# Kernel optimization log

Hardware: AMD Instinct MI355X
Metric: run time of the kernel (lower is better)

Reference implementation:

```python
import jax, jax.numpy as jnp
import numpy as np

N_MC = 32
DT = 0.1
HIDDEN = 64
PROSPECTIVE_STEPS = 3
# scan_steps=3 -> first 3 of the hard-coded velocities
VELOCITIES = np.array([[0.2, 0.0], [0.0, 0.2], [0.15, 0.15]], dtype=np.float32)


def linear_interp_1d(x, out_size):
    """F.interpolate(mode='linear', align_corners=False) on last axis. x: [..., N]."""
    n = x.shape[-1]
    scale = n / out_size
    pos = (jnp.arange(out_size, dtype=x.dtype) + 0.5) * scale - 0.5
    pos = jnp.clip(pos, 0.0, n - 1)
    lo = jnp.floor(pos).astype(jnp.int32)
    hi = jnp.minimum(lo + 1, n - 1)
    w = pos - lo.astype(x.dtype)
    return x[..., lo] * (1.0 - w) + x[..., hi] * w


def setup_inputs() -> dict:
    key = jax.random.key(0)
    ks = jax.random.split(key, 8)
    B = 16384
    image = jax.random.uniform(ks[0], (B, 28, 28), dtype=jnp.float32)
    s = 1.0 / np.sqrt(N_MC)
    W_ff = jax.random.normal(ks[1], (N_MC, N_MC), dtype=jnp.float32) * s
    W_fb = jax.random.normal(ks[2], (N_MC, N_MC), dtype=jnp.float32) * s
    W_vel = jax.random.normal(ks[3], (N_MC, 2), dtype=jnp.float32) * s
    Wc1 = jax.random.normal(ks[4], (HIDDEN, 4 * N_MC), dtype=jnp.float32) * (1.0 / np.sqrt(4 * N_MC))
    bc1 = jnp.zeros((HIDDEN,), dtype=jnp.float32)
    Wc2 = jax.random.normal(ks[5], (10, HIDDEN), dtype=jnp.float32) * (1.0 / np.sqrt(HIDDEN))
    bc2 = jnp.zeros((10,), dtype=jnp.float32)
    return {"image": image, "W_ff": W_ff, "W_fb": W_fb, "W_vel": W_vel,
            "Wc1": Wc1, "bc1": bc1, "Wc2": Wc2, "bc2": bc2}


def _column_features(image, W_ff, W_fb, W_vel):
    B = image.shape[0]
    flat = image.reshape(B, -1)                       # [B, 784]
    flat_t = jnp.swapaxes(image, 1, 2).reshape(B, -1)  # transpose(0,1) per image
    sensory = linear_interp_1d(flat, N_MC) * 80.0     # [B, n_mc]
    topdown = linear_interp_1d(flat_t, N_MC) * 40.0   # [B, n_mc]

    r6 = jnp.zeros_like(sensory)                      # reset_state per image
    y_fb = jax.nn.relu(topdown @ W_fb.T)              # top-down feedback drive
    for v in VELOCITIES:                              # fixed 3-step scan
        vel_in = W_vel @ jnp.asarray(v)               # [n_mc]
        for _ in range(PROSPECTIVE_STEPS):            # fixed 3 prospective steps
            pred = r6 @ W_fb.T                        # top-down prediction of sensory drive
            eps_pos = jax.nn.relu(sensory - pred)
            eps_neg = jax.nn.relu(pred - sensory)
            y_ff = jax.nn.relu((eps_pos - eps_neg) @ W_ff.T)
            r6 = r6 + DT * (-r6 + y_ff + y_fb + vel_in)  # leaky L6 integrator
    feature = jnp.concatenate([y_ff, y_fb, r6, eps_pos + eps_neg], axis=-1)  # [B, 4*n_mc]
    return feature


def reference(image, W_ff, W_fb, W_vel, Wc1, bc1, Wc2, bc2):
    feature = jax.lax.stop_gradient(_column_features(image, W_ff, W_fb, W_vel))
    h = jax.nn.gelu(feature @ Wc1.T + bc1, approximate=False)
    logits = h @ Wc2.T + bc2                          # [B, 10]
    return logits
```

## Files before the change

### kernel.cpp

```cpp
#include <hip/hip_runtime.h>
#include <math.h>

typedef float f32x4 __attribute__((ext_vector_type(4)));
typedef float f32x2 __attribute__((ext_vector_type(2)));

#define DOT4(A, B) ((A)[0]*(B)[0] + (A)[1]*(B)[1] + (A)[2]*(B)[2] + (A)[3]*(B)[3])

__global__ __launch_bounds__(256, 4) void mnist_dp3(
    const float* __restrict__ img, const float* __restrict__ Wff,
    const float* __restrict__ Wfb, const float* __restrict__ Wvel,
    const float* __restrict__ Wc1, const float* __restrict__ bc1,
    const float* __restrict__ Wc2, const float* __restrict__ bc2,
    float* __restrict__ out) {
  __shared__ float WffL[32 * 36];
  __shared__ float WfbL[32 * 36];
  __shared__ float uSc[2048];
  __shared__ float snL[8 * 36];
  __shared__ float tdL[8 * 36];
  __shared__ float r6L[8 * 36];
  __shared__ float ftL[8 * 132];
  __shared__ float hLd[8 * 68];
  __shared__ float Wc2L[10 * 68];

  const int t = threadIdx.x;
  const int s = t >> 5, p = t & 31;
  const int sg = blockIdx.x * 8 + s;

  const float pos = 24.5f * (float)p + 11.75f;
  const int lo = (int)pos;
  const float w = pos - (float)lo;
  const int ta = (lo % 28) * 28 + lo / 28;
  const int tb = ((lo + 1) % 28) * 28 + (lo + 1) / 28;
  const float* im = img + (size_t)sg * 784;
  const float a0 = im[lo], a1 = im[lo + 1];
  const float c0 = im[ta], c1 = im[tb];
  const float2 wvp = ((const float2*)Wvel)[p];

  {
    const int rj = t >> 3, c4 = (t & 7) * 4;
    *(f32x4*)(WffL + rj * 36 + c4) = *(const f32x4*)(Wff + rj * 32 + c4);
    *(f32x4*)(WfbL + rj * 36 + c4) = *(const f32x4*)(Wfb + rj * 32 + c4);
  }
  if (t < 160) {
    const int r2 = t >> 4, c2 = (t & 15) * 4;
    *(f32x4*)(Wc2L + r2 * 68 + c2) = *(const f32x4*)(Wc2 + r2 * 64 + c2);
  }
  const float sv = (a0 + (a1 - a0) * w) * 80.0f;
  const float tv = (c0 + (c1 - c0) * w) * 40.0f;
  snL[s * 36 + p] = sv;
  tdL[s * 36 + p] = tv;
  __syncthreads();

  {
    const int i = t >> 3, k0 = (t & 7) * 4;
    float m0 = 0.f, m1 = 0.f, m2 = 0.f, m3 = 0.f;
#pragma unroll
    for (int j = 0; j < 32; ++j) {
      const float a = WffL[i * 36 + j];
      const f32x4 w4 = *(const f32x4*)(WfbL + j * 36 + k0);
      m0 += a * w4[0]; m1 += a * w4[1]; m2 += a * w4[2]; m3 += a * w4[3];
    }
    f32x4 m = {m0, m1, m2, m3};
    *(f32x4*)(uSc + i * 36 + k0) = m;
  }
  __syncthreads();

  const float* Mrow = uSc + p * 36;
  const f32x4 M0 = *(const f32x4*)(Mrow +  0);
  const f32x4 M1 = *(const f32x4*)(Mrow +  4);
  const f32x4 M2 = *(const f32x4*)(Mrow +  8);
  const f32x4 M3 = *(const f32x4*)(Mrow + 12);
  const f32x4 M4 = *(const f32x4*)(Mrow + 16);
  const f32x4 M5 = *(const f32x4*)(Mrow + 20);
  const f32x4 M6 = *(const f32x4*)(Mrow + 24);
  const f32x4 M7 = *(const f32x4*)(Mrow + 28);

  float sf = 0.f, yb = 0.f;
#pragma unroll
  for (int jb = 0; jb < 8; ++jb) {
    const f32x4 s4 = *(const f32x4*)(snL + s * 36 + jb * 4);
    const f32x4 t4 = *(const f32x4*)(tdL + s * 36 + jb * 4);
    const f32x4 f4 = *(const f32x4*)(WffL + p * 36 + jb * 4);
    const f32x4 g4 = *(const f32x4*)(WfbL + p * 36 + jb * 4);
    sf += DOT4(f4, s4);
    yb += DOT4(g4, t4);
  }
  yb = fmaxf(yb, 0.f);

  float r = 0.f, y = 0.f, e = 0.f;
  const float VX[3] = {0.2f, 0.0f, 0.15f};
  const float VY[3] = {0.0f, 0.2f, 0.15f};
#pragma unroll
  for (int v = 0; v < 3; ++v) {
    const float vi = wvp.x * VX[v] + wvp.y * VY[v];
#pragma unroll
    for (int st = 0; st < 3; ++st) {
      r6L[s * 36 + p] = r;
      __builtin_amdgcn_wave_barrier();
      const f32x4 r40 = *(const f32x4*)(r6L + s * 36 +  0);
      const f32x4 r41 = *(const f32x4*)(r6L + s * 36 +  4);
      const f32x4 r42 = *(const f32x4*)(r6L + s * 36 +  8);
      const f32x4 r43 = *(const f32x4*)(r6L + s * 36 + 12);
      const f32x4 r44 = *(const f32x4*)(r6L + s * 36 + 16);
      const f32x4 r45 = *(const f32x4*)(r6L + s * 36 + 20);
      const f32x4 r46 = *(const f32x4*)(r6L + s * 36 + 24);
      const f32x4 r47 = *(const f32x4*)(r6L + s * 36 + 28);
      float accA = sf - DOT4(M0, r40) - DOT4(M2, r42) - DOT4(M4, r44) - DOT4(M6, r46);
      float accB =      DOT4(M1, r41) + DOT4(M3, r43) + DOT4(M5, r45) + DOT4(M7, r47);
      if (v == 2 && st == 2) {
        float pa = 0.f, pb = 0.f;
        const float* gr = WfbL + p * 36;
        pa += DOT4((*(const f32x4*)(gr +  0)), r40);
        pb += DOT4((*(const f32x4*)(gr +  4)), r41);
        pa += DOT4((*(const f32x4*)(gr +  8)), r42);
        pb += DOT4((*(const f32x4*)(gr + 12)), r43);
        pa += DOT4((*(const f32x4*)(gr + 16)), r44);
        pb += DOT4((*(const f32x4*)(gr + 20)), r45);
        pa += DOT4((*(const f32x4*)(gr + 24)), r46);
        pb += DOT4((*(const f32x4*)(gr + 28)), r47);
        e = fabsf(sv - (pa + pb));
      }
      __builtin_amdgcn_wave_barrier();
      y = fmaxf(accA - accB, 0.f);
      r += 0.1f * (y - r + yb + vi);
    }
  }

  ftL[s * 132 +      p] = y;
  ftL[s * 132 + 32 + p] = yb;
  ftL[s * 132 + 64 + p] = r;
  ftL[s * 132 + 96 + p] = e;
  __syncthreads();

  {
    const int q = t >> 6, o = t & 63;
    const float* wrow = Wc1 + (size_t)o * 128 + q * 32;
    float acc[8] = {0.f, 0.f, 0.f, 0.f, 0.f, 0.f, 0.f, 0.f};
#pragma unroll
    for (int fb = 0; fb < 8; ++fb) {
      const f32x4 w4 = *(const f32x4*)(wrow + fb * 4);
#pragma unroll
      for (int ss = 0; ss < 8; ++ss) {
        const f32x4 f4 = *(const f32x4*)(ftL + ss * 132 + q * 32 + fb * 4);
        acc[ss] += DOT4(w4, f4);
      }
    }
#pragma unroll
    for (int ss = 0; ss < 8; ++ss)
      uSc[q * 512 + ss * 64 + o] = acc[ss];
  }
  __syncthreads();

  {
    const int o = t & 63, s2 = t >> 6;
    const float b = bc1[o];
    const float hA = b + uSc[s2 * 64 + o]        + uSc[512 + s2 * 64 + o]
                       + uSc[1024 + s2 * 64 + o] + uSc[1536 + s2 * 64 + o];
    const int s3 = s2 + 4;
    const float hB = b + uSc[s3 * 64 + o]        + uSc[512 + s3 * 64 + o]
                       + uSc[1024 + s3 * 64 + o] + uSc[1536 + s3 * 64 + o];
    hLd[s2 * 68 + o] = 0.5f * hA * (1.0f + erff(hA * 0.70710678118654752f));
    hLd[s3 * 68 + o] = 0.5f * hB * (1.0f + erff(hB * 0.70710678118654752f));
  }
  __syncthreads();

  if (p < 10) {
    float acc = bc2[p];
    const float* w2 = Wc2L + p * 68;
#pragma unroll
    for (int hb = 0; hb < 16; ++hb) {
      const f32x4 h4 = *(const f32x4*)(hLd + s * 68 + hb * 4);
      const f32x4 w4 = *(const f32x4*)(w2 + hb * 4);
      acc += DOT4(w4, h4);
    }
    out[(size_t)sg * 10 + p] = acc;
  }
}

extern "C" void kernel_launch(void* const* d_in, const int* in_sizes, int n_in,
                              void* d_out, int out_size, void* d_ws, size_t ws_size,
                              hipStream_t stream) {
  const float* img  = (const float*)d_in[0];
  const float* Wff  = (const float*)d_in[1];
  const float* Wfb  = (const float*)d_in[2];
  const float* Wvel = (const float*)d_in[3];
  const float* Wc1  = (const float*)d_in[4];
  const float* bc1  = (const float*)d_in[5];
  const float* Wc2  = (const float*)d_in[6];
  const float* bc2  = (const float*)d_in[7];
  float* out = (float*)d_out;
  const int B = in_sizes[0] / 784;
  const int grid = B / 8;
  hipLaunchKernelGGL(mnist_dp3, dim3(grid), dim3(256), 0, stream,
                     img, Wff, Wfb, Wvel, Wc1, bc1, Wc2, bc2, out);
}
```

Measured before the change: 27.96 us.

## Stage images and Wc1 through shared memory with coalesced vector loads

Each block now loads its 8 images with coalesced float4 loads into a large shared buffer, instead of making 4 scattered global loads per thread. The Wc1 weights are prefetched into registers before the recurrence loop and then written into the same reused shared buffer for the classifier matmul. Wc2 is read straight from global memory rather than staged, and the launch bounds no longer force 4 blocks per CU. The risk is lower occupancy, because each block now uses roughly 34KB more LDS and holds more registers live, and it now pulls the whole image into the chip instead of the few sampled values.

After: 38.03 us. 1.36x slower.

```diff
diff --git a/kernel.cpp b/kernel.cpp
--- a/kernel.cpp
+++ b/kernel.cpp
@@ -6,50 +6,64 @@
 
 #define DOT4(A, B) ((A)[0]*(B)[0] + (A)[1]*(B)[1] + (A)[2]*(B)[2] + (A)[3]*(B)[3])
 
-__global__ __launch_bounds__(256, 4) void mnist_dp3(
+__global__ __launch_bounds__(256) void mnist_dp4(
     const float* __restrict__ img, const float* __restrict__ Wff,
     const float* __restrict__ Wfb, const float* __restrict__ Wvel,
     const float* __restrict__ Wc1, const float* __restrict__ bc1,
     const float* __restrict__ Wc2, const float* __restrict__ bc2,
     float* __restrict__ out) {
+  __shared__ float A[64 * 132];
   __shared__ float WffL[32 * 36];
   __shared__ float WfbL[32 * 36];
-  __shared__ float uSc[2048];
+  __shared__ float Bu[2048];
   __shared__ float snL[8 * 36];
   __shared__ float tdL[8 * 36];
   __shared__ float r6L[8 * 36];
   __shared__ float ftL[8 * 132];
   __shared__ float hLd[8 * 68];
-  __shared__ float Wc2L[10 * 68];
 
   const int t = threadIdx.x;
   const int s = t >> 5, p = t & 31;
   const int sg = blockIdx.x * 8 + s;
+
+  const float* gimg = img + (size_t)blockIdx.x * 8 * 784;
+  f32x4 i0 = *(const f32x4*)(gimg + (t)          * 4);
+  f32x4 i1 = *(const f32x4*)(gimg + (t + 256)    * 4);
+  f32x4 i2 = *(const f32x4*)(gimg + (t + 512)    * 4);
+  f32x4 i3 = *(const f32x4*)(gimg + (t + 768)    * 4);
+  f32x4 i4 = *(const f32x4*)(gimg + (t + 1024)   * 4);
+  f32x4 i5 = *(const f32x4*)(gimg + (t + 1280)   * 4);
+  f32x4 i6 = {0.f, 0.f, 0.f, 0.f};
+  if (t < 32) i6 = *(const f32x4*)(gimg + (t + 1536) * 4);
+
+  const int rj = t >> 3, c4 = (t & 7) * 4;
+  const f32x4 wf4 = *(const f32x4*)(Wff + rj * 32 + c4);
+  const f32x4 wb4 = *(const f32x4*)(Wfb + rj * 32 + c4);
+  const float2 wvp = ((const float2*)Wvel)[p];
+
+  *(f32x4*)(WffL + rj * 36 + c4) = wf4;
+  *(f32x4*)(WfbL + rj * 36 + c4) = wb4;
+  *(f32x4*)(A + (t)          * 4) = i0;
+  *(f32x4*)(A + (t + 256)    * 4) = i1;
+  *(f32x4*)(A + (t + 512)    * 4) = i2;
+  *(f32x4*)(A + (t + 768)    * 4) = i3;
+  *(f32x4*)(A + (t + 1024)   * 4) = i4;
+  *(f32x4*)(A + (t + 1280)   * 4) = i5;
+  if (t < 32) *(f32x4*)(A + (t + 1536) * 4) = i6;
+  __syncthreads();
 
   const float pos = 24.5f * (float)p + 11.75f;
   const int lo = (int)pos;
   const float w = pos - (float)lo;
   const int ta = (lo % 28) * 28 + lo / 28;
   const int tb = ((lo + 1) % 28) * 28 + (lo + 1) / 28;
-  const float* im = img + (size_t)sg * 784;
-  const float a0 = im[lo], a1 = im[lo + 1];
-  const float c0 = im[ta], c1 = im[tb];
-  const float2 wvp = ((const float2*)Wvel)[p];
-
-  {
-    const int rj = t >> 3, c4 = (t & 7) * 4;
-    *(f32x4*)(WffL + rj * 36 + c4) = *(const f32x4*)(Wff + rj * 32 + c4);
-    *(f32x4*)(WfbL + rj * 36 + c4) = *(const f32x4*)(Wfb + rj * 32 + c4);
-  }
-  if (t < 160) {
-    const int r2 = t >> 4, c2 = (t & 15) * 4;
-    *(f32x4*)(Wc2L + r2 * 68 + c2) = *(const f32x4*)(Wc2 + r2 * 64 + c2);
-  }
+  const float* ims = A + s * 784;
+  const float a0 = ims[lo], a1 = ims[lo + 1];
+  const float c0 = ims[ta], c1 = ims[tb];
   const float sv = (a0 + (a1 - a0) * w) * 80.0f;
   const float tv = (c0 + (c1 - c0) * w) * 40.0f;
   snL[s * 36 + p] = sv;
   tdL[s * 36 + p] = tv;
-  __syncthreads();
 
   {
     const int i = t >> 3, k0 = (t & 7) * 4;
@@ -61,11 +75,11 @@
       m0 += a * w4[0]; m1 += a * w4[1]; m2 += a * w4[2]; m3 += a * w4[3];
     }
     f32x4 m = {m0, m1, m2, m3};
-    *(f32x4*)(uSc + i * 36 + k0) = m;
-  }
-  __syncthreads();
-
-  const float* Mrow = uSc + p * 36;
+    *(f32x4*)(Bu + i * 36 + k0) = m;
+  }
+  __syncthreads();
+
+  const float* Mrow = Bu + p * 36;
   const f32x4 M0 = *(const f32x4*)(Mrow +  0);
   const f32x4 M1 = *(const f32x4*)(Mrow +  4);
   const f32x4 M2 = *(const f32x4*)(Mrow +  8);
@@ -86,6 +100,15 @@
     yb += DOT4(g4, t4);
   }
   yb = fmaxf(yb, 0.f);
+
+  f32x4 cw0 = *(const f32x4*)(Wc1 + (t)          * 4);
+  f32x4 cw1 = *(const f32x4*)(Wc1 + (t + 256)    * 4);
+  f32x4 cw2 = *(const f32x4*)(Wc1 + (t + 512)    * 4);
+  f32x4 cw3 = *(const f32x4*)(Wc1 + (t + 768)    * 4);
+  f32x4 cw4 = *(const f32x4*)(Wc1 + (t + 1024)   * 4);
+  f32x4 cw5 = *(const f32x4*)(Wc1 + (t + 1280)   * 4);
+  f32x4 cw6 = *(const f32x4*)(Wc1 + (t + 1536)   * 4);
+  f32x4 cw7 = *(const f32x4*)(Wc1 + (t + 1792)   * 4);
 
   float r = 0.f, y = 0.f, e = 0.f;
   const float VX[3] = {0.2f, 0.0f, 0.15f};
@@ -126,6 +149,17 @@
     }
   }
 
+  {
+    const int u0 = t;
+    *(f32x4*)(A + (u0 >> 5) * 132 + (u0 & 31) * 4)          = cw0;
+    *(f32x4*)(A + ((u0 + 256)  >> 5) * 132 + (u0 & 31) * 4) = cw1;
+    *(f32x4*)(A + ((u0 + 512)  >> 5) * 132 + (u0 & 31) * 4) = cw2;
+    *(f32x4*)(A + ((u0 + 768)  >> 5) * 132 + (u0 & 31) * 4) = cw3;
+    *(f32x4*)(A + ((u0 + 1024) >> 5) * 132 + (u0 & 31) * 4) = cw4;
+    *(f32x4*)(A + ((u0 + 1280) >> 5) * 132 + (u0 & 31) * 4) = cw5;
+    *(f32x4*)(A + ((u0 + 1536) >> 5) * 132 + (u0 & 31) * 4) = cw6;
+    *(f32x4*)(A + ((u0 + 1792) >> 5) * 132 + (u0 & 31) * 4) = cw7;
+  }
   ftL[s * 132 +      p] = y;
   ftL[s * 132 + 32 + p] = yb;
   ftL[s * 132 + 64 + p] = r;
@@ -134,7 +168,7 @@
 
   {
     const int q = t >> 6, o = t & 63;
-    const float* wrow = Wc1 + (size_t)o * 128 + q * 32;
+    const float* wrow = A + o * 132 + q * 32;
     float acc[8] = {0.f, 0.f, 0.f, 0.f, 0.f, 0.f, 0.f, 0.f};
 #pragma unroll
     for (int fb = 0; fb < 8; ++fb) {
@@ -147,18 +181,18 @@
     }
 #pragma unroll
     for (int ss = 0; ss < 8; ++ss)
-      uSc[q * 512 + ss * 64 + o] = acc[ss];
+      Bu[q * 512 + ss * 64 + o] = acc[ss];
   }
   __syncthreads();
 
   {
     const int o = t & 63, s2 = t >> 6;
     const float b = bc1[o];
-    const float hA = b + uSc[s2 * 64 + o]        + uSc[512 + s2 * 64 + o]
-                       + uSc[1024 + s2 * 64 + o] + uSc[1536 + s2 * 64 + o];
+    const float hA = b + Bu[s2 * 64 + o]        + Bu[512 + s2 * 64 + o]
+                       + Bu[1024 + s2 * 64 + o] + Bu[1536 + s2 * 64 + o];
     const int s3 = s2 + 4;
-    const float hB = b + uSc[s3 * 64 + o]        + uSc[512 + s3 * 64 + o]
-                       + uSc[1024 + s3 * 64 + o] + uSc[1536 + s3 * 64 + o];
+    const float hB = b + Bu[s3 * 64 + o]        + Bu[512 + s3 * 64 + o]
+                       + Bu[1024 + s3 * 64 + o] + Bu[1536 + s3 * 64 + o];
     hLd[s2 * 68 + o] = 0.5f * hA * (1.0f + erff(hA * 0.70710678118654752f));
     hLd[s3 * 68 + o] = 0.5f * hB * (1.0f + erff(hB * 0.70710678118654752f));
   }
@@ -166,7 +200,7 @@
 
   if (p < 10) {
     float acc = bc2[p];
-    const float* w2 = Wc2L + p * 68;
+    const float* w2 = Wc2 + (size_t)p * 64;
 #pragma unroll
     for (int hb = 0; hb < 16; ++hb) {
       const f32x4 h4 = *(const f32x4*)(hLd + s * 68 + hb * 4);
@@ -191,6 +225,6 @@
   float* out = (float*)d_out;
   const int B = in_sizes[0] / 784;
   const int grid = B / 8;
-  hipLaunchKernelGGL(mnist_dp3, dim3(grid), dim3(256), 0, stream,
+  hipLaunchKernelGGL(mnist_dp4, dim3(grid), dim3(256), 0, stream,
                      img, Wff, Wfb, Wvel, Wc1, bc1, Wc2, bc2, out);
 }
```
